# Kernel optimization log

Hardware: AMD Instinct MI355X
Metric: run time of the kernel (lower is better)

The kernel has to match this reference:

```python
import jax, jax.numpy as jnp
import numpy as np

BN_EPS = 1e-5


def _lin(key, fan_in, fan_out):
    k1, k2 = jax.random.split(key)
    s = 1.0 / np.sqrt(fan_in)
    w = jax.random.uniform(k1, (fan_in, fan_out), jnp.float32, -s, s)
    b = jax.random.uniform(k2, (fan_out,), jnp.float32, -s, s)
    return w, b


def setup_inputs() -> dict:
    key = jax.random.key(0)
    ks = jax.random.split(key, 24)
    N, E, F_IN, E_DIM, G = 50000, 800000, 64, 16, 128
    inp = {}
    inp["x"] = jax.random.normal(ks[0], (N, F_IN), jnp.float32)
    inp["edge_attr"] = jax.random.normal(ks[1], (E, E_DIM), jnp.float32)
    inp["edge_index"] = jax.random.randint(ks[2], (2, E), 0, N, jnp.int64)
    inp["batch_ids"] = jnp.sort(jax.random.randint(ks[3], (N,), 0, G, jnp.int64))
    # conv1: edge lin (16->64), mlp 64->256->256
    inp["we1"], inp["be1"] = _lin(ks[4], E_DIM, F_IN)
    inp["w1a"], inp["b1a"] = _lin(ks[5], F_IN, 256)
    inp["w1b"], inp["b1b"] = _lin(ks[6], 256, 256)
    inp["bn1_g"] = jnp.ones((256,), jnp.float32)
    inp["bn1_b"] = jnp.zeros((256,), jnp.float32)
    inp["bn1_m"] = 0.1 * jax.random.normal(ks[7], (256,), jnp.float32)
    inp["bn1_v"] = jnp.abs(jax.random.normal(ks[8], (256,), jnp.float32)) + 0.5
    # conv2: edge lin (16->256), mlp 256->128->128
    inp["we2"], inp["be2"] = _lin(ks[9], E_DIM, 256)
    inp["w2a"], inp["b2a"] = _lin(ks[10], 256, 128)
    inp["w2b"], inp["b2b"] = _lin(ks[11], 128, 128)
    inp["bn2_g"] = jnp.ones((128,), jnp.float32)
    inp["bn2_b"] = jnp.zeros((128,), jnp.float32)
    inp["bn2_m"] = 0.1 * jax.random.normal(ks[12], (128,), jnp.float32)
    inp["bn2_v"] = jnp.abs(jax.random.normal(ks[13], (128,), jnp.float32)) + 0.5
    # conv3: edge lin (16->128), mlp 128->64->64
    inp["we3"], inp["be3"] = _lin(ks[14], E_DIM, 128)
    inp["w3a"], inp["b3a"] = _lin(ks[15], 128, 64)
    inp["w3b"], inp["b3b"] = _lin(ks[16], 64, 64)
    inp["bn3_g"] = jnp.ones((64,), jnp.float32)
    inp["bn3_b"] = jnp.zeros((64,), jnp.float32)
    inp["bn3_m"] = 0.1 * jax.random.normal(ks[17], (64,), jnp.float32)
    inp["bn3_v"] = jnp.abs(jax.random.normal(ks[18], (64,), jnp.float32)) + 0.5
    inp["fc1_w"], inp["fc1_b"] = _lin(ks[19], 64, 16)
    inp["fc2_w"], inp["fc2_b"] = _lin(ks[20], 16, 1)
    return inp


def _gine(x, edge_index, edge_attr, we, be, wa, ba, wb, bb):
    # GINEConv, eps=0: mlp(x + sum_j relu(x_j + lin_e(e_ji)))
    src, dst = edge_index[0], edge_index[1]
    msg = jax.nn.relu(x[src] + edge_attr @ we + be)  # [E, d]
    agg = jax.ops.segment_sum(msg, dst, num_segments=x.shape[0])
    h = x + agg
    return jax.nn.relu(h @ wa + ba) @ wb + bb


def _bn(x, g, b, m, v):
    return (x - m) * jax.lax.rsqrt(v + BN_EPS) * g + b


def reference(x, edge_attr, edge_index, batch_ids,
              we1, be1, w1a, b1a, w1b, b1b, bn1_g, bn1_b, bn1_m, bn1_v,
              we2, be2, w2a, b2a, w2b, b2b, bn2_g, bn2_b, bn2_m, bn2_v,
              we3, be3, w3a, b3a, w3b, b3b, bn3_g, bn3_b, bn3_m, bn3_v,
              fc1_w, fc1_b, fc2_w, fc2_b):
    G = 128  # num graphs
    h = _gine(x, edge_index, edge_attr, we1, be1, w1a, b1a, w1b, b1b)
    h = _bn(jax.nn.relu(h), bn1_g, bn1_b, bn1_m, bn1_v)
    h = _gine(h, edge_index, edge_attr, we2, be2, w2a, b2a, w2b, b2b)
    h = _bn(jax.nn.relu(h), bn2_g, bn2_b, bn2_m, bn2_v)
    h = _gine(h, edge_index, edge_attr, we3, be3, w3a, b3a, w3b, b3b)
    h = _bn(jax.nn.relu(h), bn3_g, bn3_b, bn3_m, bn3_v)
    pooled = jax.ops.segment_sum(h, batch_ids, num_segments=G)  # [G, 64]
    out = jax.nn.relu(pooled @ fc1_w + fc1_b) @ fc2_w + fc2_b  # [G, 1]
    return out
```

## Files before the change

kernel.cpp:

```cpp
#include <hip/hip_runtime.h>
#include <hip/hip_bf16.h>

#define BN_EPS 1e-5f

typedef __attribute__((ext_vector_type(8))) short short8v;
typedef __attribute__((ext_vector_type(4))) float f32x4;
typedef _Float16 f16x2 __attribute__((ext_vector_type(2)));
typedef __hip_bfloat16 bf16;
typedef unsigned short ushort_t;
typedef unsigned int uint_t;

__global__ void count_kernel(const int* __restrict__ dst, int* __restrict__ deg,
                             int E, int N) {
    int i = blockIdx.x * blockDim.x + threadIdx.x;
    if (i >= E) return;
    int d = dst[i];
    d = min(max(d, 0), N - 1);
    atomicAdd(&deg[d], 1);
}

__global__ __launch_bounds__(256) void scan1_kernel(const int* __restrict__ deg,
                                                    int* __restrict__ bsum, int N) {
    int t = threadIdx.x, b = blockIdx.x;
    int i = b * 256 + t;
    int v = (i < N) ? deg[i] : 0;
#pragma unroll
    for (int d = 32; d; d >>= 1) v += __shfl_xor(v, d, 64);
    __shared__ int ws[4];
    if ((t & 63) == 0) ws[t >> 6] = v;
    __syncthreads();
    if (t == 0) bsum[b] = ws[0] + ws[1] + ws[2] + ws[3];
}

__global__ __launch_bounds__(256) void scan3_kernel(const int* __restrict__ deg,
                                                    const int* __restrict__ bsum,
                                                    int* __restrict__ off,
                                                    int* __restrict__ cur,
                                                    int N, int nb) {
    int t = threadIdx.x, b = blockIdx.x;
    int lane = t & 63, w = t >> 6;

    int partial = 0;
    for (int j = t; j < b; j += 256) partial += bsum[j];
#pragma unroll
    for (int d = 32; d; d >>= 1) partial += __shfl_xor(partial, d, 64);
    __shared__ int bsm[4];
    if (lane == 0) bsm[w] = partial;
    __syncthreads();
    int base = bsm[0] + bsm[1] + bsm[2] + bsm[3];

    int i = b * 256 + t;
    int v = (i < N) ? deg[i] : 0;
    int inc = v;
#pragma unroll
    for (int d = 1; d < 64; d <<= 1) {
        int u = __shfl_up(inc, d, 64);
        if (lane >= d) inc += u;
    }
    __shared__ int ws[4];
    if (lane == 63) ws[w] = inc;
    __syncthreads();
    for (int j = 0; j < w; ++j) base += ws[j];
    int excl = base + inc - v;
    if (i < N) { off[i] = excl; cur[i] = excl; }
    if (i == N - 1) off[N] = excl + v;
}

__global__ void fill_kernel(const int* __restrict__ src, const int* __restrict__ dst,
                            const float* __restrict__ ea, int* __restrict__ cur,
                            int* __restrict__ srcs, uint_t* __restrict__ each,
                            int E, int N) {
    int i = blockIdx.x * blockDim.x + threadIdx.x;
    if (i >= E) return;
    int d = dst[i];
    d = min(max(d, 0), N - 1);
    int p = atomicAdd(&cur[d], 1);
    srcs[p] = min(max(src[i], 0), N - 1);
    uint_t pk[8];
#pragma unroll
    for (int q = 0; q < 4; ++q) {
        float4 a = *(const float4*)&ea[(size_t)i * 16 + q * 4];
        f16x2 h0 = {(_Float16)a.x, (_Float16)a.y};
        f16x2 h1 = {(_Float16)a.z, (_Float16)a.w};
        pk[q * 2 + 0] = __builtin_bit_cast(uint_t, h0);
        pk[q * 2 + 1] = __builtin_bit_cast(uint_t, h1);
    }
    *(uint4*)&each[(size_t)p * 8 + 0] = *(uint4*)&pk[0];
    *(uint4*)&each[(size_t)p * 8 + 4] = *(uint4*)&pk[4];
}

__global__ void megaconv_kernel(
    const float* __restrict__ x, bf16* __restrict__ xb, int nx4,
    const float* __restrict__ w1a, const float* __restrict__ w1b,
    const float* __restrict__ w2a, const float* __restrict__ w2b,
    const float* __restrict__ w3a, const float* __restrict__ w3b,
    bf16* __restrict__ wt,
    const float* __restrict__ we1, const float* __restrict__ we2,
    const float* __restrict__ we3, uint_t* __restrict__ wef,
    int* __restrict__ deg, int N, float* __restrict__ pooled) {
    int t = blockIdx.x * blockDim.x + threadIdx.x;
    if (t < nx4) {
        int i = t * 4;
        float4 v = *(const float4*)&x[i];
        xb[i + 0] = __float2bfloat16(v.x);
        xb[i + 1] = __float2bfloat16(v.y);
        xb[i + 2] = __float2bfloat16(v.z);
        xb[i + 3] = __float2bfloat16(v.w);
        return;
    }
    t -= nx4;
    if (t < 143360) {
        const float* w; int K, Nc, base, r;
        if (t < 16384)       { w = w1a; K = 64;  Nc = 256; base = 0;      r = t; }
        else if (t < 81920)  { w = w1b; K = 256; Nc = 256; base = 16384;  r = t - 16384; }
        else if (t < 114688) { w = w2a; K = 256; Nc = 128; base = 81920;  r = t - 81920; }
        else if (t < 131072) { w = w2b; K = 128; Nc = 128; base = 114688; r = t - 114688; }
        else if (t < 139264) { w = w3a; K = 128; Nc = 64;  base = 131072; r = t - 131072; }
        else                 { w = w3b; K = 64;  Nc = 64;  base = 139264; r = t - 139264; }
        int ktn = K / 32;
        int j = r & 7;
        int lane = (r >> 3) & 63;
        int rem = r >> 9;
        int kt = rem % ktn;
        int nt = rem / ktn;
        int col = nt * 16 + (lane & 15);
        int k = kt * 32 + ((lane >> 4) << 3) + j;
        wt[base + r] = __float2bfloat16(w[(size_t)k * Nc + col]);
        return;
    }
    t -= 143360;
    if (t < 3584) {
        const float* w; int D, base, r;
        if (t < 512)        { w = we1; D = 64;  base = 0;    r = t; }
        else if (t < 2560)  { w = we2; D = 256; base = 512;  r = t - 512; }
        else                { w = we3; D = 128; base = 2560; r = t - 2560; }
        int p = r / D, col = r % D;
        f16x2 h = {(_Float16)w[(size_t)(2 * p) * D + col],
                   (_Float16)w[(size_t)(2 * p + 1) * D + col]};
        wef[base + r] = __builtin_bit_cast(uint_t, h);
        return;
    }
    t -= 3584;
    {
        int nd4 = (N + 3) / 4;
        if (t < nd4) {
            int i = t * 4;
#pragma unroll
            for (int j = 0; j < 4; ++j)
                if (i + j < N) deg[i + j] = 0;
            return;
        }
        t -= nd4;
        if (t < 2048) {
            *(float4*)&pooled[t * 4] = make_float4(0.f, 0.f, 0.f, 0.f);
        }
    }
}

template <int C>
__global__ __launch_bounds__(256) void msg_fused(
    const uint_t* __restrict__ each, const int* __restrict__ srcs,
    const int* __restrict__ off, const bf16* __restrict__ x,
    const uint_t* __restrict__ wef, const float* __restrict__ be,
    bf16* __restrict__ t, int N) {
    constexpr int D = C * 64;
    const int lane = threadIdx.x & 63;
    const int n = blockIdx.x * 4 + (threadIdx.x >> 6);
    if (n >= N) return;
    const int col0 = lane * C;

    uint_t wreg[8][C];
#pragma unroll
    for (int p = 0; p < 8; ++p)
#pragma unroll
        for (int c = 0; c < C; ++c) wreg[p][c] = wef[p * D + col0 + c];
    float breg[C];
#pragma unroll
    for (int c = 0; c < C; ++c) breg[c] = be[col0 + c];

    float acc[C];
#pragma unroll
    for (int c = 0; c < C; ++c) acc[c] = 0.f;

    const ushort_t* xp = (const ushort_t*)x;

    const int i0 = __builtin_amdgcn_readfirstlane(off[n]);
    const int i1 = __builtin_amdgcn_readfirstlane(off[n + 1]);

#define BF2F(u) (__builtin_bit_cast(float, (unsigned)(u) << 16))
#define H2(u) (__builtin_bit_cast(f16x2, u))

    int i = i0;
    int sN[4] = {0, 0, 0, 0};
    if (i + 4 <= i1) {
#pragma unroll
        for (int j = 0; j < 4; ++j)
            sN[j] = __builtin_amdgcn_readfirstlane(srcs[i + j]);
    }
    for (; i + 4 <= i1; i += 4) {
        int s[4];
#pragma unroll
        for (int j = 0; j < 4; ++j) s[j] = sN[j];
        ushort_t xv[4][C];
#pragma unroll
        for (int j = 0; j < 4; ++j) {
            if constexpr (C == 4) {
                *(ushort4*)xv[j] = *(const ushort4*)&xp[(size_t)s[j] * D + col0];
            } else if constexpr (C == 2) {
                *(ushort2*)xv[j] = *(const ushort2*)&xp[(size_t)s[j] * D + col0];
            } else {
                xv[j][0] = xp[(size_t)s[j] * D + col0];
            }
        }
        if (i + 8 <= i1) {
#pragma unroll
            for (int j = 0; j < 4; ++j)
                sN[j] = __builtin_amdgcn_readfirstlane(srcs[i + 4 + j]);
        }
        uint_t e[4][8];
#pragma unroll
        for (int j = 0; j < 4; ++j)
#pragma unroll
            for (int p = 0; p < 8; ++p) e[j][p] = each[(size_t)(i + j) * 8 + p];

        float m[4][C];
#pragma unroll
        for (int j = 0; j < 4; ++j)
#pragma unroll
            for (int c = 0; c < C; ++c)
                m[j][c] = __builtin_amdgcn_fdot2(H2(e[j][0]), H2(wreg[0][c]), breg[c], false);
#pragma unroll
        for (int p = 1; p < 8; ++p)
#pragma unroll
            for (int j = 0; j < 4; ++j)
#pragma unroll
                for (int c = 0; c < C; ++c)
                    m[j][c] = __builtin_amdgcn_fdot2(H2(e[j][p]), H2(wreg[p][c]), m[j][c], false);
#pragma unroll
        for (int j = 0; j < 4; ++j)
#pragma unroll
            for (int c = 0; c < C; ++c)
                acc[c] += fmaxf(m[j][c] + BF2F(xv[j][c]), 0.f);
    }
    for (; i < i1; ++i) {
        const int s0 = __builtin_amdgcn_readfirstlane(srcs[i]);
        ushort_t xv0[C];
        if constexpr (C == 4) {
            *(ushort4*)xv0 = *(const ushort4*)&xp[(size_t)s0 * D + col0];
        } else if constexpr (C == 2) {
            *(ushort2*)xv0 = *(const ushort2*)&xp[(size_t)s0 * D + col0];
        } else {
            xv0[0] = xp[(size_t)s0 * D + col0];
        }
        uint_t e0[8];
#pragma unroll
        for (int p = 0; p < 8; ++p) e0[p] = each[(size_t)i * 8 + p];
        float m0[C];
#pragma unroll
        for (int c = 0; c < C; ++c)
            m0[c] = __builtin_amdgcn_fdot2(H2(e0[0]), H2(wreg[0][c]), breg[c], false);
#pragma unroll
        for (int p = 1; p < 8; ++p)
#pragma unroll
            for (int c = 0; c < C; ++c)
                m0[c] = __builtin_amdgcn_fdot2(H2(e0[p]), H2(wreg[p][c]), m0[c], false);
#pragma unroll
        for (int c = 0; c < C; ++c) acc[c] += fmaxf(m0[c] + BF2F(xv0[c]), 0.f);
    }

#pragma unroll
    for (int c = 0; c < C; ++c) {
        float xo = BF2F(xp[(size_t)n * D + col0 + c]);
        t[(size_t)n * D + col0 + c] = __float2bfloat16(xo + acc[c]);
    }
#undef BF2F
#undef H2
}

template <int NC>
__global__ __launch_bounds__(256) void gemm64(
    const bf16* __restrict__ A, const bf16* __restrict__ Wp_,
    const float* __restrict__ bias, const float* __restrict__ bng,
    const float* __restrict__ bnb, const float* __restrict__ bnm,
    const float* __restrict__ bnv, bf16* __restrict__ C,
    const int* __restrict__ batch, float* __restrict__ pooled,
    int M, int K, int mode) {
    const int lane = threadIdx.x & 63;
    const int w = threadIdx.x >> 6;
    const int r16 = lane & 15;
    const int kg = lane >> 4;
    const int mbase = blockIdx.x * 256 + w * 64;
    const int nbase = blockIdx.y * 64;
    const int ktn = K >> 5;

    f32x4 acc[4][4];
#pragma unroll
    for (int f = 0; f < 4; ++f)
#pragma unroll
        for (int nt = 0; nt < 4; ++nt) acc[f][nt] = (f32x4){0.f, 0.f, 0.f, 0.f};

    const short* Ap = (const short*)A;
    const short* Wp = (const short*)Wp_;

    for (int kt = 0; kt < ktn; ++kt) {
        short8v b[4];
#pragma unroll
        for (int nt = 0; nt < 4; ++nt)
            b[nt] = *(const short8v*)&Wp[(((size_t)(blockIdx.y * 4 + nt) * ktn + kt) * 64 + lane) * 8];
        short8v a[4];
#pragma unroll
        for (int f = 0; f < 4; ++f)
            a[f] = *(const short8v*)&Ap[(size_t)(mbase + f * 16 + r16) * K + kt * 32 + kg * 8];
#pragma unroll
        for (int f = 0; f < 4; ++f)
#pragma unroll
            for (int nt = 0; nt < 4; ++nt)
                acc[f][nt] = __builtin_amdgcn_mfma_f32_16x16x32_bf16(a[f], b[nt], acc[f][nt], 0, 0, 0);
    }

    float bs[4], sc[4], sh[4];
#pragma unroll
    for (int nt = 0; nt < 4; ++nt) {
        int col = nbase + nt * 16 + r16;
        bs[nt] = bias[col];
        sc[nt] = 1.f; sh[nt] = 0.f;
        if (mode >= 2) {
            sc[nt] = rsqrtf(bnv[col] + BN_EPS) * bng[col];
            sh[nt] = bnb[col] - bnm[col] * sc[nt];
        }
    }

#pragma unroll
    for (int f = 0; f < 4; ++f) {
#pragma unroll
        for (int rg = 0; rg < 4; ++rg) {
            int row = mbase + f * 16 + kg * 4 + rg;
            if (row >= M) continue;
            int g = 0;
            if (mode == 3) g = min(max(batch[row], 0), 127);
#pragma unroll
            for (int nt = 0; nt < 4; ++nt) {
                int col = nbase + nt * 16 + r16;
                float z = acc[f][nt][rg] + bs[nt];
                z = fmaxf(z, 0.f);
                if (mode >= 2) z = z * sc[nt] + sh[nt];
                if (mode == 3)
                    atomicAdd(&pooled[g * NC + col], z);
                else
                    C[(size_t)row * NC + col] = __float2bfloat16(z);
            }
        }
    }
}

__global__ __launch_bounds__(128) void head_kernel(
    const float* __restrict__ pooled, const float* __restrict__ w1,
    const float* __restrict__ b1, const float* __restrict__ w2,
    const float* __restrict__ b2, float* __restrict__ out) {
    const int g = threadIdx.x;
    float p[64];
#pragma unroll
    for (int i = 0; i < 64; ++i) p[i] = pooled[g * 64 + i];
    float o = b2[0];
#pragma unroll
    for (int j = 0; j < 16; ++j) {
        float hsum = b1[j];
#pragma unroll
        for (int i = 0; i < 64; ++i) hsum = fmaf(p[i], w1[i * 16 + j], hsum);
        o = fmaf(fmaxf(hsum, 0.f), w2[j], o);
    }
    out[g] = o;
}

extern "C" void kernel_launch(void* const* d_in, const int* in_sizes, int n_in,
                              void* d_out, int out_size, void* d_ws,
                              size_t ws_size, hipStream_t stream) {
    const float* x     = (const float*)d_in[0];
    const float* ea    = (const float*)d_in[1];
    const int*   ei    = (const int*)d_in[2];
    const int*   batch = (const int*)d_in[3];
    const float* we1 = (const float*)d_in[4];
    const float* be1 = (const float*)d_in[5];
    const float* w1a = (const float*)d_in[6];
    const float* b1a = (const float*)d_in[7];
    const float* w1b = (const float*)d_in[8];
    const float* b1b = (const float*)d_in[9];
    const float* bn1g = (const float*)d_in[10];
    const float* bn1b = (const float*)d_in[11];
    const float* bn1m = (const float*)d_in[12];
    const float* bn1v = (const float*)d_in[13];
    const float* we2 = (const float*)d_in[14];
    const float* be2 = (const float*)d_in[15];
    const float* w2a = (const float*)d_in[16];
    const float* b2a = (const float*)d_in[17];
    const float* w2b = (const float*)d_in[18];
    const float* b2b = (const float*)d_in[19];
    const float* bn2g = (const float*)d_in[20];
    const float* bn2b = (const float*)d_in[21];
    const float* bn2m = (const float*)d_in[22];
    const float* bn2v = (const float*)d_in[23];
    const float* we3 = (const float*)d_in[24];
    const float* be3 = (const float*)d_in[25];
    const float* w3a = (const float*)d_in[26];
    const float* b3a = (const float*)d_in[27];
    const float* w3b = (const float*)d_in[28];
    const float* b3b = (const float*)d_in[29];
    const float* bn3g = (const float*)d_in[30];
    const float* bn3b = (const float*)d_in[31];
    const float* bn3m = (const float*)d_in[32];
    const float* bn3v = (const float*)d_in[33];
    const float* fc1w = (const float*)d_in[34];
    const float* fc1b = (const float*)d_in[35];
    const float* fc2w = (const float*)d_in[36];
    const float* fc2b = (const float*)d_in[37];

    const int N = in_sizes[0] / 64;
    const int E = in_sizes[1] / 16;
    const int M_pad = ((N + 255) / 256) * 256;
    const int* src = ei;
    const int* dst = ei + E;

    char* wsp = (char*)d_ws;
    auto alloc = [&](size_t bytes) -> void* {
        void* p = (void*)wsp;
        wsp += (bytes + 255) & ~(size_t)255;
        return p;
    };
    const int nb = (N + 255) / 256;
    int* deg    = (int*)alloc((size_t)N * 4);
    int* off    = (int*)alloc((size_t)(N + 1) * 4);
    int* cur    = (int*)alloc((size_t)N * 4);
    int* bsum   = (int*)alloc((size_t)nb * 4);
    int* srcs   = (int*)alloc((size_t)E * 4);
    uint_t* each = (uint_t*)alloc((size_t)E * 8 * 4);
    bf16* xb    = (bf16*)alloc((size_t)M_pad * 64 * 2);
    bf16* tb    = (bf16*)alloc((size_t)M_pad * 256 * 2);
    bf16* ub    = (bf16*)alloc((size_t)M_pad * 256 * 2);
    bf16* hb    = (bf16*)alloc((size_t)M_pad * 256 * 2);
    bf16* wt    = (bf16*)alloc((size_t)143360 * 2);
    uint_t* wef = (uint_t*)alloc((size_t)3584 * 4);
    float* pooled = (float*)alloc(128 * 64 * 4);

    bf16* wt1a = wt + 0;
    bf16* wt1b = wt + 16384;
    bf16* wt2a = wt + 81920;
    bf16* wt2b = wt + 114688;
    bf16* wt3a = wt + 131072;
    bf16* wt3b = wt + 139264;
    uint_t* wef1 = wef + 0;
    uint_t* wef2 = wef + 512;
    uint_t* wef3 = wef + 2560;

    {
        int nx4 = N * 64 / 4;
        int total = nx4 + 143360 + 3584 + (N + 3) / 4 + 2048;
        megaconv_kernel<<<(total + 255) / 256, 256, 0, stream>>>(
            x, xb, nx4, w1a, w1b, w2a, w2b, w3a, w3b, wt, we1, we2, we3, wef,
            deg, N, pooled);
    }

    int eb = (E + 255) / 256;
    count_kernel<<<eb, 256, 0, stream>>>(dst, deg, E, N);
    scan1_kernel<<<nb, 256, 0, stream>>>(deg, bsum, N);
    scan3_kernel<<<nb, 256, 0, stream>>>(deg, bsum, off, cur, N, nb);
    fill_kernel<<<eb, 256, 0, stream>>>(src, dst, ea, cur, srcs, each, E, N);

    const int g256 = M_pad / 256;
    const int mblk = (N + 3) / 4;

    msg_fused<1><<<mblk, 256, 0, stream>>>(each, srcs, off, xb, wef1, be1, tb, N);
    gemm64<256><<<dim3(g256, 4), 256, 0, stream>>>(tb, wt1a, b1a, nullptr, nullptr,
                                                   nullptr, nullptr, ub, nullptr,
                                                   nullptr, N, 64, 1);
    gemm64<256><<<dim3(g256, 4), 256, 0, stream>>>(ub, wt1b, b1b, bn1g, bn1b, bn1m,
                                                   bn1v, hb, nullptr, nullptr,
                                                   N, 256, 2);
    msg_fused<4><<<mblk, 256, 0, stream>>>(each, srcs, off, hb, wef2, be2, tb, N);
    gemm64<128><<<dim3(g256, 2), 256, 0, stream>>>(tb, wt2a, b2a, nullptr, nullptr,
                                                   nullptr, nullptr, ub, nullptr,
                                                   nullptr, N, 256, 1);
    gemm64<128><<<dim3(g256, 2), 256, 0, stream>>>(ub, wt2b, b2b, bn2g, bn2b, bn2m,
                                                   bn2v, hb, nullptr, nullptr,
                                                   N, 128, 2);
    msg_fused<2><<<mblk, 256, 0, stream>>>(each, srcs, off, hb, wef3, be3, tb, N);
    gemm64<64><<<dim3(g256, 1), 256, 0, stream>>>(tb, wt3a, b3a, nullptr, nullptr,
                                                  nullptr, nullptr, ub, nullptr,
                                                  nullptr, N, 128, 1);
    gemm64<64><<<dim3(g256, 1), 256, 0, stream>>>(ub, wt3b, b3b, bn3g, bn3b, bn3m,
                                                  bn3v, nullptr, batch, pooled,
                                                  N, 64, 3);

    head_kernel<<<1, 128, 0, stream>>>(pooled, fc1w, fc1b, fc2w, fc2b, (float*)d_out);
}
```

Measured before the change: 410.9 us.

## Schedule message-passing waves by descending node degree for load balance

```diff
diff --git a/kernel.cpp b/kernel.cpp
--- a/kernel.cpp
+++ b/kernel.cpp
@@ -87,6 +87,35 @@
     }
     *(uint4*)&each[(size_t)p * 8 + 0] = *(uint4*)&pk[0];
     *(uint4*)&each[(size_t)p * 8 + 4] = *(uint4*)&pk[4];
+}
+
+__global__ void hist_kernel(const int* __restrict__ deg, int* __restrict__ bcnt,
+                            int N) {
+    int i = blockIdx.x * blockDim.x + threadIdx.x;
+    if (i >= N) return;
+    int b = 63 - min(deg[i], 63);
+    atomicAdd(&bcnt[b], 1);
+}
+
+__global__ __launch_bounds__(64) void hscan_kernel(int* __restrict__ bcnt) {
+    int t = threadIdx.x;
+    int v = bcnt[t];
+    int inc = v;
+#pragma unroll
+    for (int d = 1; d < 64; d <<= 1) {
+        int u = __shfl_up(inc, d, 64);
+        if (t >= d) inc += u;
+    }
+    bcnt[t] = inc - v;
+}
+
+__global__ void scatter_kernel(const int* __restrict__ deg, int* __restrict__ bcur,
+                               int* __restrict__ order, int N) {
+    int i = blockIdx.x * blockDim.x + threadIdx.x;
+    if (i >= N) return;
+    int b = 63 - min(deg[i], 63);
+    int p = atomicAdd(&bcur[b], 1);
+    order[p] = i;
 }
 
 __global__ void megaconv_kernel(
@@ -162,11 +191,12 @@
     const uint_t* __restrict__ each, const int* __restrict__ srcs,
     const int* __restrict__ off, const bf16* __restrict__ x,
     const uint_t* __restrict__ wef, const float* __restrict__ be,
-    bf16* __restrict__ t, int N) {
+    const int* __restrict__ order, bf16* __restrict__ t, int N) {
     constexpr int D = C * 64;
     const int lane = threadIdx.x & 63;
-    const int n = blockIdx.x * 4 + (threadIdx.x >> 6);
-    if (n >= N) return;
+    const int wid = blockIdx.x * 4 + (threadIdx.x >> 6);
+    if (wid >= N) return;
+    const int n = __builtin_amdgcn_readfirstlane(order[wid]);
     const int col0 = lane * C;
 
     uint_t wreg[8][C];
@@ -432,6 +462,8 @@
     int* cur    = (int*)alloc((size_t)N * 4);
     int* bsum   = (int*)alloc((size_t)nb * 4);
     int* srcs   = (int*)alloc((size_t)E * 4);
+    int* order  = (int*)alloc((size_t)N * 4);
+    int* bcnt   = (int*)alloc(64 * 4);
     uint_t* each = (uint_t*)alloc((size_t)E * 8 * 4);
     bf16* xb    = (bf16*)alloc((size_t)M_pad * 64 * 2);
     bf16* tb    = (bf16*)alloc((size_t)M_pad * 256 * 2);
@@ -458,6 +490,7 @@
             x, xb, nx4, w1a, w1b, w2a, w2b, w3a, w3b, wt, we1, we2, we3, wef,
             deg, N, pooled);
     }
+    hipMemsetAsync(bcnt, 0, 64 * 4, stream);
 
     int eb = (E + 255) / 256;
     count_kernel<<<eb, 256, 0, stream>>>(dst, deg, E, N);
@@ -465,24 +498,28 @@
     scan3_kernel<<<nb, 256, 0, stream>>>(deg, bsum, off, cur, N, nb);
     fill_kernel<<<eb, 256, 0, stream>>>(src, dst, ea, cur, srcs, each, E, N);
 
+    hist_kernel<<<nb, 256, 0, stream>>>(deg, bcnt, N);
+    hscan_kernel<<<1, 64, 0, stream>>>(bcnt);
+    scatter_kernel<<<nb, 256, 0, stream>>>(deg, bcnt, order, N);
+
     const int g256 = M_pad / 256;
     const int mblk = (N + 3) / 4;
 
-    msg_fused<1><<<mblk, 256, 0, stream>>>(each, srcs, off, xb, wef1, be1, tb, N);
+    msg_fused<1><<<mblk, 256, 0, stream>>>(each, srcs, off, xb, wef1, be1, order, tb, N);
     gemm64<256><<<dim3(g256, 4), 256, 0, stream>>>(tb, wt1a, b1a, nullptr, nullptr,
                                                    nullptr, nullptr, ub, nullptr,
                                                    nullptr, N, 64, 1);
     gemm64<256><<<dim3(g256, 4), 256, 0, stream>>>(ub, wt1b, b1b, bn1g, bn1b, bn1m,
                                                    bn1v, hb, nullptr, nullptr,
                                                    N, 256, 2);
-    msg_fused<4><<<mblk, 256, 0, stream>>>(each, srcs, off, hb, wef2, be2, tb, N);
+    msg_fused<4><<<mblk, 256, 0, stream>>>(each, srcs, off, hb, wef2, be2, order, tb, N);
     gemm64<128><<<dim3(g256, 2), 256, 0, stream>>>(tb, wt2a, b2a, nullptr, nullptr,
                                                    nullptr, nullptr, ub, nullptr,
                                                    nullptr, N, 256, 1);
     gemm64<128><<<dim3(g256, 2), 256, 0, stream>>>(ub, wt2b, b2b, bn2g, bn2b, bn2m,
                                                    bn2v, hb, nullptr, nullptr,
                                                    N, 128, 2);
-    msg_fused<2><<<mblk, 256, 0, stream>>>(each, srcs, off, hb, wef3, be3, tb, N);
+    msg_fused<2><<<mblk, 256, 0, stream>>>(each, srcs, off, hb, wef3, be3, order, tb, N);
     gemm64<64><<<dim3(g256, 1), 256, 0, stream>>>(tb, wt3a, b3a, nullptr, nullptr,
                                                   nullptr, nullptr, ub, nullptr,
                                                   nullptr, N, 128, 1);
```

Result: slower. 698.2 us (+69.9%).
